# Performance work log

Measured on AMD Instinct MI355X. Metric: run time of the kernel, lower is better.

Reference implementation:

```python
import jax, jax.numpy as jnp
import numpy as np

N, K, H = 50000, 8, 128  # nodes per level, mailbox fanout, hidden size


def setup_inputs() -> dict:
    key = jax.random.key(0)
    ks = jax.random.split(key, 16)
    s = 1.0 / np.sqrt(H)
    inp = {
        "x": jax.random.normal(ks[0], (N, H), jnp.float32),
        "h_mail": jax.random.normal(ks[1], (N, K, H), jnp.float32),
        "c_mail": jax.random.normal(ks[2], (N, K, H), jnp.float32),
        "Wiou": jax.random.uniform(ks[3], (H, 3 * H), jnp.float32, -s, s),
        "Uiou": jax.random.uniform(ks[4], (2 * H, 3 * H), jnp.float32, -s, s),
        "biou": jnp.zeros((1, 3 * H), jnp.float32),
        "Of": jax.random.uniform(ks[5], (H, H), jnp.float32, -s, s),
        "Zf": jax.random.uniform(ks[6], (H, H), jnp.float32, -s, s),
        "Qf": jax.random.uniform(ks[7], (H, H), jnp.float32, -s, s),
        "Kf": jax.random.uniform(ks[8], (H, H), jnp.float32, -s, s),
        "vf": jax.random.uniform(ks[9], (H, H), jnp.float32, -s, s),
        "Wa": jax.random.uniform(ks[10], (H, H), jnp.float32, -s, s),
        "Wd": jax.random.uniform(ks[11], (H, H), jnp.float32, -s, s),
        "Vf": jax.random.uniform(ks[12], (H, 1), jnp.float32, -s, s),
        "etype": jax.random.randint(ks[13], (N, K), 0, 2, jnp.int32),
    }
    return inp


def reference(x, h_mail, c_mail, Wiou, Uiou, biou, Of, Zf, Qf, Kf, vf, Wa, Wd, Vf, etype):
    # --- message: mailbox of child h, c and edge type e (0/1) ---
    e = etype.astype(x.dtype)[..., None]                     # [N,K,1]
    # --- reduce_func ---
    x_tild = x @ Wiou                                        # W_iou(features) -> iou  [N,3H]
    n_tild = x @ Qf                                          # [N,H]
    hk = h_mail @ Kf                                         # K_f(h_tild) [N,K,H]
    v_tild = hk @ vf                                         # [N,K,H]
    w = jax.nn.softmax(jnp.tanh((n_tild[:, None, :] + hk) @ Vf), axis=1)  # [N,K,1]
    modify = jnp.mean(e, axis=1)                             # sum(et)/K  [N,1]
    score_a = (1.0 - modify)[:, None, :]                     # [N,1,1]
    score_b = modify[:, None, :]
    h_til1 = jnp.sum(w * score_a * e * (v_tild @ Wa), axis=1)        # [N,H]
    h_til0 = jnp.sum(w * score_b * (1.0 - e) * (v_tild @ Wd), axis=1)
    h_tild = jnp.concatenate([h_til0, h_til1], axis=1)       # [N,2H]
    f = jax.nn.sigmoid((h_mail * e) @ Of + (h_mail * (1.0 - e)) @ Zf)
    c_red = jnp.sum(f * c_mail, axis=1)                      # [N,H]
    iou = h_tild @ Uiou + x_tild                             # [N,3H]
    # --- apply_node_func ---
    iou = iou + biou
    i, o, u = jnp.split(iou, 3, axis=1)
    i, o, u = jax.nn.sigmoid(i), jax.nn.sigmoid(o), jnp.tanh(u)
    c = i * u + c_red
    h = o * jnp.tanh(c)
    return jnp.stack([h, c])                                 # [2,N,H]
```

## Files before the change

### kernel.cpp

```cpp
#include <hip/hip_runtime.h>
#include <math.h>

#define NN 50000
#define HH 128
#define KK 8

#define WS_WTF  0
#define WS_BT   16384
#define WS_KV   90112
#define WS_T0   106496
#define WS_T1   122880
#define WS_kv   139264
#define WS_qv   139392

typedef __attribute__((ext_vector_type(8))) unsigned short u16x8;
typedef __attribute__((ext_vector_type(8))) __bf16 bf16x8;
typedef __attribute__((ext_vector_type(4))) float f32x4;
union Frag { u16x8 u; bf16x8 b; };

__device__ __forceinline__ unsigned short f2bf(float f) {
    unsigned u = __builtin_bit_cast(unsigned, f);
    u += 0x7fffu + ((u >> 16) & 1u);
    return (unsigned short)(u >> 16);
}
__device__ __forceinline__ float sigm(float v) { return 1.f / (1.f + expf(-v)); }

#define GF(row, slot) ((row) * 128 + ((((slot) ^ ((row) & 7))) << 3))

__global__ void prepA(const float* __restrict__ Kf, const float* __restrict__ Qf,
                      const float* __restrict__ vf, const float* __restrict__ Vf,
                      const float* __restrict__ Wiou, const float* __restrict__ Of,
                      const float* __restrict__ Zf, float* __restrict__ ws) {
    int idx = blockIdx.x * 256 + threadIdx.x;
    unsigned short* bt = (unsigned short*)(ws + WS_BT);
    if (idx < 16384) {
        int a = idx >> 7, c = idx & 127;
        float s = 0.f;
        for (int b = 0; b < 128; ++b) s += Kf[a * 128 + b] * vf[b * 128 + c];
        ws[WS_KV + idx] = s;
    } else if (idx < 16512) {
        int a = idx - 16384;
        float s = 0.f;
        for (int b = 0; b < 128; ++b) s += Kf[a * 128 + b] * Vf[b];
        ws[WS_kv + a] = s;
    } else if (idx < 16640) {
        int a = idx - 16512;
        float s = 0.f;
        for (int b = 0; b < 128; ++b) s += Qf[a * 128 + b] * Vf[b];
        ws[WS_qv + a] = s;
    } else if (idx < 65792) {
        int i = idx - 16640;
        int r = i / 384, c = i % 384;
        bt[c * 384 + r] = f2bf(Wiou[i]);
    } else {
        int i = idx - 65792;
        int c = i >> 8, k = i & 255;
        float v = (k < 128) ? Of[k * 128 + c] : Zf[(k - 128) * 128 + c];
        unsigned short* wtf = (unsigned short*)(ws + WS_WTF);
        wtf[i] = f2bf(v);
    }
}

__global__ void prep2(const float* __restrict__ Wd, const float* __restrict__ Wa,
                      float* __restrict__ ws) {
    int idx = blockIdx.x * 256 + threadIdx.x;
    int sel = idx >> 14;
    int r = (idx >> 7) & 127, c = idx & 127;
    const float* W = sel ? Wa : Wd;
    const float* Kv = ws + WS_KV;
    float s = 0.f;
    for (int h = 0; h < 128; ++h) s += Kv[r * 128 + h] * W[h * 128 + c];
    ws[(sel ? WS_T1 : WS_T0) + r * 128 + c] = s;
}

__global__ void prep3(const float* __restrict__ Uiou, float* __restrict__ ws) {
    int idx = blockIdx.x * 256 + threadIdx.x;
    int half = (idx >= 49152) ? 1 : 0;
    int i2 = idx - half * 49152;
    int r = i2 / 384, c = i2 % 384;
    const float* T = ws + (half ? WS_T1 : WS_T0);
    const float* U = Uiou + half * 128 * 384;
    float s = 0.f;
    for (int h = 0; h < 128; ++h) s += T[r * 128 + h] * U[h * 384 + c];
    unsigned short* bt = (unsigned short*)(ws + WS_BT);
    bt[c * 384 + (128 + half * 128 + r)] = f2bf(s);
}

__global__ __launch_bounds__(256) __attribute__((amdgpu_waves_per_eu(4, 4)))
void tree_main(
    const float* __restrict__ x, const float* __restrict__ h_mail,
    const float* __restrict__ c_mail, const float* __restrict__ biou,
    const int* __restrict__ etype, const float* __restrict__ ws,
    float* __restrict__ out)
{
    __shared__ unsigned short GfS[48 * 128];
    __shared__ float credS[16 * 132];
    __shared__ float efS[128];

    const int t = threadIdx.x;
    const int node0 = blockIdx.x * 16;

    {
        const int n = t >> 4, s = t & 15, c0 = s * 8;
        const int node = node0 + n;
        if (t < 128) efS[t] = (float)etype[node0 * KK + t];

        float xv[8];
        const float4* xp = (const float4*)(x + node * HH + c0);
        float4 x0 = xp[0], x1 = xp[1];
        xv[0]=x0.x; xv[1]=x0.y; xv[2]=x0.z; xv[3]=x0.w;
        xv[4]=x1.x; xv[5]=x1.y; xv[6]=x1.z; xv[7]=x1.w;
        u16x8 xg;
        #pragma unroll
        for (int j = 0; j < 8; ++j) xg[j] = f2bf(xv[j]);
        *(u16x8*)(&GfS[GF(s, n)]) = xg;

        const float4* kvp = (const float4*)(ws + WS_kv + c0);
        float4 k0 = kvp[0], k1 = kvp[1];
        const float4* qvp = (const float4*)(ws + WS_qv + c0);
        float4 q0 = qvp[0], q1 = qvp[1];
        float kvv[8] = {k0.x,k0.y,k0.z,k0.w,k1.x,k1.y,k1.z,k1.w};
        float qvv[8] = {q0.x,q0.y,q0.z,q0.w,q1.x,q1.y,q1.z,q1.w};
        __syncthreads();

        float xq = 0.f;
        #pragma unroll
        for (int j = 0; j < 8; ++j) xq += xv[j] * qvv[j];

        float p[KK];
        #pragma unroll
        for (int k = 0; k < KK; ++k) {
            const float4* hp = (const float4*)(h_mail + (node * KK + k) * HH + c0);
            float4 h0 = hp[0], h1 = hp[1];
            p[k] = h0.x*kvv[0] + h0.y*kvv[1] + h0.z*kvv[2] + h0.w*kvv[3]
                 + h1.x*kvv[4] + h1.y*kvv[5] + h1.z*kvv[6] + h1.w*kvv[7];
        }
        #pragma unroll
        for (int msk = 8; msk >= 1; msk >>= 1) {
            xq += __shfl_xor(xq, msk, 16);
            #pragma unroll
            for (int k = 0; k < KK; ++k) p[k] += __shfl_xor(p[k], msk, 16);
        }
        float ef[KK], esum = 0.f;
        #pragma unroll
        for (int k = 0; k < KK; ++k) { ef[k] = efS[n * KK + k]; esum += ef[k]; }
        const float mod = esum * 0.125f;
        const float sa = 1.f - mod, sb = mod;

        float tk[KK], mx = -1e30f;
        #pragma unroll
        for (int k = 0; k < KK; ++k) { tk[k] = tanhf(xq + p[k]); mx = fmaxf(mx, tk[k]); }
        float wsum = 0.f;
        #pragma unroll
        for (int k = 0; k < KK; ++k) { tk[k] = expf(tk[k] - mx); wsum += tk[k]; }
        const float inv = 1.f / wsum;
        float cf0[KK], cf1[KK];
        #pragma unroll
        for (int k = 0; k < KK; ++k) {
            float w = tk[k] * inv;
            cf0[k] = sb * w * (1.f - ef[k]);
            cf1[k] = sa * w * ef[k];
        }
        float a0[8] = {0,0,0,0,0,0,0,0}, a1[8] = {0,0,0,0,0,0,0,0};
        #pragma unroll
        for (int k = 0; k < KK; ++k) {
            const float4* hp = (const float4*)(h_mail + (node * KK + k) * HH + c0);
            float4 h0 = hp[0], h1 = hp[1];
            float hv[8];
            hv[0]=h0.x; hv[1]=h0.y; hv[2]=h0.z; hv[3]=h0.w;
            hv[4]=h1.x; hv[5]=h1.y; hv[6]=h1.z; hv[7]=h1.w;
            #pragma unroll
            for (int j = 0; j < 8; ++j) { a0[j] += cf0[k]*hv[j]; a1[j] += cf1[k]*hv[j]; }
        }
        u16x8 g0, g1;
        #pragma unroll
        for (int j = 0; j < 8; ++j) { g0[j] = f2bf(a0[j]); g1[j] = f2bf(a1[j]); }
        *(u16x8*)(&GfS[GF(16 + s, n)]) = g0;
        *(u16x8*)(&GfS[GF(32 + s, n)]) = g1;
    }
    __syncthreads();

    const int wave = t >> 6, lane = t & 63, m = lane & 15, q = lane >> 4;
    {
        const unsigned short* WtF = (const unsigned short*)(ws + WS_WTF);
        f32x4 acc[2][8];
        #pragma unroll
        for (int rt = 0; rt < 2; ++rt)
            #pragma unroll
            for (int tc = 0; tc < 8; ++tc) acc[rt][tc] = (f32x4){0.f,0.f,0.f,0.f};

        #pragma unroll
        for (int ks = 0; ks < 8; ++ks) {
            const int kg = ks * 32 + q * 8;
            Frag bf[8], af[2];
            #pragma unroll
            for (int tc = 0; tc < 8; ++tc)
                bf[tc].u = *(const u16x8*)(WtF + (tc * 16 + m) * 256 + kg);
            #pragma unroll
            for (int rt = 0; rt < 2; ++rt) {
                const int r = wave * 32 + rt * 16 + m;
                const float msk = (ks < 4) ? efS[r] : (1.f - efS[r]);
                const float4* hp = (const float4*)(h_mail + (node0 * KK + r) * HH + (kg & 127));
                float4 h0 = hp[0], h1 = hp[1];
                float tv[8];
                tv[0]=h0.x*msk; tv[1]=h0.y*msk; tv[2]=h0.z*msk; tv[3]=h0.w*msk;
                tv[4]=h1.x*msk; tv[5]=h1.y*msk; tv[6]=h1.z*msk; tv[7]=h1.w*msk;
                #pragma unroll
                for (int j = 0; j < 8; ++j) af[rt].u[j] = f2bf(tv[j]);
            }
            #pragma unroll
            for (int rt = 0; rt < 2; ++rt)
                #pragma unroll
                for (int tc = 0; tc < 8; ++tc)
                    acc[rt][tc] = __builtin_amdgcn_mfma_f32_16x16x32_bf16(
                        af[rt].b, bf[tc].b, acc[rt][tc], 0, 0, 0);
        }
        #pragma unroll
        for (int rt = 0; rt < 2; ++rt) {
            const int rbase = wave * 32 + rt * 16;
            const float* cp = c_mail + (node0 * KK + rbase + q * 4) * HH + m;
            float cm[8][4];
            #pragma unroll
            for (int tc = 0; tc < 8; ++tc)
                #pragma unroll
                for (int reg = 0; reg < 4; ++reg)
                    cm[tc][reg] = cp[reg * HH + tc * 16];
            #pragma unroll
            for (int tc = 0; tc < 8; ++tc) {
                float sacc = 0.f;
                #pragma unroll
                for (int reg = 0; reg < 4; ++reg)
                    sacc += sigm(acc[rt][tc][reg]) * cm[tc][reg];
                sacc += __shfl_xor(sacc, 16);
                if ((q & 1) == 0) {
                    const int nl = (rbase >> 3) + (q >> 1);
                    credS[nl * 132 + tc * 16 + m] = sacc;
                }
            }
        }
    }

    f32x4 acc2[6];
    {
        const unsigned short* Bt = (const unsigned short*)(ws + WS_BT);
        #pragma unroll
        for (int j = 0; j < 6; ++j) acc2[j] = (f32x4){0.f,0.f,0.f,0.f};
        #pragma unroll
        for (int ks = 0; ks < 12; ++ks) {
            const int kg = ks * 32 + q * 8;
            const int row = kg >> 3;
            Frag ag;
            ag.u = *(const u16x8*)(&GfS[GF(row, m)]);
            #pragma unroll
            for (int j = 0; j < 6; ++j) {
                const int tile = (j >> 1) * 8 + wave * 2 + (j & 1);
                Frag bg;
                bg.u = *(const u16x8*)(Bt + (tile * 16 + m) * 384 + kg);
                acc2[j] = __builtin_amdgcn_mfma_f32_16x16x32_bf16(
                    ag.b, bg.b, acc2[j], 0, 0, 0);
            }
        }
    }
    __syncthreads();

    {
        #pragma unroll
        for (int jj = 0; jj < 2; ++jj) {
            const int c = (wave * 2 + jj) * 16 + m;
            const float bi = biou[c];
            const float bo = biou[128 + c];
            const float bu = biou[256 + c];
            #pragma unroll
            for (int reg = 0; reg < 4; ++reg) {
                const int n = q * 4 + reg;
                const float ii = sigm(acc2[jj][reg] + bi);
                const float oo = sigm(acc2[2 + jj][reg] + bo);
                const float uu = tanhf(acc2[4 + jj][reg] + bu);
                const float cc = ii * uu + credS[n * 132 + c];
                out[(node0 + n) * HH + c] = oo * tanhf(cc);
                out[NN * HH + (node0 + n) * HH + c] = cc;
            }
        }
    }
}

extern "C" void kernel_launch(void* const* d_in, const int* in_sizes, int n_in,
                              void* d_out, int out_size, void* d_ws, size_t ws_size,
                              hipStream_t stream) {
    const float* x      = (const float*)d_in[0];
    const float* h_mail = (const float*)d_in[1];
    const float* c_mail = (const float*)d_in[2];
    const float* Uiou   = (const float*)d_in[4];
    const float* biou   = (const float*)d_in[5];
    const float* Of     = (const float*)d_in[6];
    const float* Zf     = (const float*)d_in[7];
    const float* Qf     = (const float*)d_in[8];
    const float* Kf     = (const float*)d_in[9];
    const float* vf     = (const float*)d_in[10];
    const float* Wa     = (const float*)d_in[11];
    const float* Wd     = (const float*)d_in[12];
    const float* Vf     = (const float*)d_in[13];
    const int*   etype  = (const int*)d_in[14];
    const float* Wiou   = (const float*)d_in[3];
    float* ws  = (float*)d_ws;
    float* out = (float*)d_out;

    hipLaunchKernelGGL(prepA, dim3(385), dim3(256), 0, stream, Kf, Qf, vf, Vf, Wiou, Of, Zf, ws);
    hipLaunchKernelGGL(prep2, dim3(128), dim3(256), 0, stream, Wd, Wa, ws);
    hipLaunchKernelGGL(prep3, dim3(384), dim3(256), 0, stream, Uiou, ws);
    hipLaunchKernelGGL(tree_main, dim3(3125), dim3(256), 0, stream,
                       x, h_mail, c_mail, biou, etype, ws, out);
}
```

Measured before the change: 884.1 us.

## Fuse three weight-prep kernels into one block-redundant prep kernel and relax main occupancy

Replaces the three chained weight-preparation launches with a single 48-block kernel. Each block recomputes the Kf·vf product into shared memory, multiplies it by Wd or Wa, then produces its own column slice of the folded Uiou weights. This removes two launches and the round trips through global scratch, at the cost of redundant per-block matmul work on few blocks. It also drops the waves_per_eu(4,4) attribute on the main kernel and interleaves the c_mail loads with their use to lower register pressure.

```diff
diff --git a/kernel.cpp b/kernel.cpp
--- a/kernel.cpp
+++ b/kernel.cpp
@@ -7,9 +7,6 @@
 
 #define WS_WTF  0
 #define WS_BT   16384
-#define WS_KV   90112
-#define WS_T0   106496
-#define WS_T1   122880
 #define WS_kv   139264
 #define WS_qv   139392
 
@@ -27,67 +24,78 @@
 
 #define GF(row, slot) ((row) * 128 + ((((slot) ^ ((row) & 7))) << 3))
 
-__global__ void prepA(const float* __restrict__ Kf, const float* __restrict__ Qf,
-                      const float* __restrict__ vf, const float* __restrict__ Vf,
-                      const float* __restrict__ Wiou, const float* __restrict__ Of,
-                      const float* __restrict__ Zf, float* __restrict__ ws) {
-    int idx = blockIdx.x * 256 + threadIdx.x;
-    unsigned short* bt = (unsigned short*)(ws + WS_BT);
-    if (idx < 16384) {
-        int a = idx >> 7, c = idx & 127;
+__global__ __launch_bounds__(512) void prep_all(
+    const float* __restrict__ Kf, const float* __restrict__ Qf,
+    const float* __restrict__ vf, const float* __restrict__ Vf,
+    const float* __restrict__ Wiou, const float* __restrict__ Of,
+    const float* __restrict__ Zf, const float* __restrict__ Wd,
+    const float* __restrict__ Wa, const float* __restrict__ Uiou,
+    float* __restrict__ ws)
+{
+    __shared__ float KVs[128 * 128];
+    const int t = threadIdx.x;
+    const int bh = blockIdx.x;
+    const int half = (bh >= 24) ? 1 : 0;
+    const int cb = (bh % 24) * 16;
+    unsigned short* bt  = (unsigned short*)(ws + WS_BT);
+    unsigned short* wtf = (unsigned short*)(ws + WS_WTF);
+
+    for (int idx = bh * 512 + t; idx < 82176; idx += 48 * 512) {
+        if (idx < 128) {
+            float s = 0.f;
+            for (int b = 0; b < 128; ++b) s += Kf[idx * 128 + b] * Vf[b];
+            ws[WS_kv + idx] = s;
+        } else if (idx < 256) {
+            int a = idx - 128;
+            float s = 0.f;
+            for (int b = 0; b < 128; ++b) s += Qf[a * 128 + b] * Vf[b];
+            ws[WS_qv + a] = s;
+        } else if (idx < 49408) {
+            int i = idx - 256;
+            int r = i / 384, c = i % 384;
+            bt[c * 384 + r] = f2bf(Wiou[i]);
+        } else {
+            int i = idx - 49408;
+            int c = i >> 8, k = i & 255;
+            float v = (k < 128) ? Of[k * 128 + c] : Zf[(k - 128) * 128 + c];
+            wtf[i] = f2bf(v);
+        }
+    }
+
+    for (int i = t; i < 16384; i += 512) {
+        int a = i >> 7, c = i & 127;
         float s = 0.f;
         for (int b = 0; b < 128; ++b) s += Kf[a * 128 + b] * vf[b * 128 + c];
-        ws[WS_KV + idx] = s;
-    } else if (idx < 16512) {
-        int a = idx - 16384;
+        KVs[i] = s;
+    }
+    __syncthreads();
+
+    const float* W = half ? Wa : Wd;
+    float treg[32];
+    #pragma unroll
+    for (int j = 0; j < 32; ++j) {
+        int i = t + j * 512;
+        int r = i >> 7, h = i & 127;
         float s = 0.f;
-        for (int b = 0; b < 128; ++b) s += Kf[a * 128 + b] * Vf[b];
-        ws[WS_kv + a] = s;
-    } else if (idx < 16640) {
-        int a = idx - 16512;
+        for (int g = 0; g < 128; ++g) s += KVs[r * 128 + g] * W[g * 128 + h];
+        treg[j] = s;
+    }
+    __syncthreads();
+    #pragma unroll
+    for (int j = 0; j < 32; ++j) KVs[t + j * 512] = treg[j];
+    __syncthreads();
+
+    const float* U = Uiou + half * 128 * 384;
+    for (int i = t; i < 128 * 16; i += 512) {
+        int r = i >> 4, cc = i & 15;
+        int c = cb + cc;
         float s = 0.f;
-        for (int b = 0; b < 128; ++b) s += Qf[a * 128 + b] * Vf[b];
-        ws[WS_qv + a] = s;
-    } else if (idx < 65792) {
-        int i = idx - 16640;
-        int r = i / 384, c = i % 384;
-        bt[c * 384 + r] = f2bf(Wiou[i]);
-    } else {
-        int i = idx - 65792;
-        int c = i >> 8, k = i & 255;
-        float v = (k < 128) ? Of[k * 128 + c] : Zf[(k - 128) * 128 + c];
-        unsigned short* wtf = (unsigned short*)(ws + WS_WTF);
-        wtf[i] = f2bf(v);
+        for (int h = 0; h < 128; ++h) s += KVs[r * 128 + h] * U[h * 384 + c];
+        bt[c * 384 + (128 + half * 128 + r)] = f2bf(s);
     }
 }
 
-__global__ void prep2(const float* __restrict__ Wd, const float* __restrict__ Wa,
-                      float* __restrict__ ws) {
-    int idx = blockIdx.x * 256 + threadIdx.x;
-    int sel = idx >> 14;
-    int r = (idx >> 7) & 127, c = idx & 127;
-    const float* W = sel ? Wa : Wd;
-    const float* Kv = ws + WS_KV;
-    float s = 0.f;
-    for (int h = 0; h < 128; ++h) s += Kv[r * 128 + h] * W[h * 128 + c];
-    ws[(sel ? WS_T1 : WS_T0) + r * 128 + c] = s;
-}
-
-__global__ void prep3(const float* __restrict__ Uiou, float* __restrict__ ws) {
-    int idx = blockIdx.x * 256 + threadIdx.x;
-    int half = (idx >= 49152) ? 1 : 0;
-    int i2 = idx - half * 49152;
-    int r = i2 / 384, c = i2 % 384;
-    const float* T = ws + (half ? WS_T1 : WS_T0);
-    const float* U = Uiou + half * 128 * 384;
-    float s = 0.f;
-    for (int h = 0; h < 128; ++h) s += T[r * 128 + h] * U[h * 384 + c];
-    unsigned short* bt = (unsigned short*)(ws + WS_BT);
-    bt[c * 384 + (128 + half * 128 + r)] = f2bf(s);
-}
-
-__global__ __launch_bounds__(256) __attribute__((amdgpu_waves_per_eu(4, 4)))
-void tree_main(
+__global__ __launch_bounds__(256) void tree_main(
     const float* __restrict__ x, const float* __restrict__ h_mail,
     const float* __restrict__ c_mail, const float* __restrict__ biou,
     const int* __restrict__ etype, const float* __restrict__ ws,
@@ -219,18 +227,16 @@
         for (int rt = 0; rt < 2; ++rt) {
             const int rbase = wave * 32 + rt * 16;
             const float* cp = c_mail + (node0 * KK + rbase + q * 4) * HH + m;
-            float cm[8][4];
-            #pragma unroll
-            for (int tc = 0; tc < 8; ++tc)
+            #pragma unroll
+            for (int tc = 0; tc < 8; ++tc) {
+                float cm[4];
                 #pragma unroll
                 for (int reg = 0; reg < 4; ++reg)
-                    cm[tc][reg] = cp[reg * HH + tc * 16];
-            #pragma unroll
-            for (int tc = 0; tc < 8; ++tc) {
+                    cm[reg] = cp[reg * HH + tc * 16];
                 float sacc = 0.f;
                 #pragma unroll
                 for (int reg = 0; reg < 4; ++reg)
-                    sacc += sigm(acc[rt][tc][reg]) * cm[tc][reg];
+                    sacc += sigm(acc[rt][tc][reg]) * cm[reg];
                 sacc += __shfl_xor(sacc, 16);
                 if ((q & 1) == 0) {
                     const int nl = (rbase >> 3) + (q >> 1);
@@ -290,6 +296,7 @@
     const float* x      = (const float*)d_in[0];
     const float* h_mail = (const float*)d_in[1];
     const float* c_mail = (const float*)d_in[2];
+    const float* Wiou   = (const float*)d_in[3];
     const float* Uiou   = (const float*)d_in[4];
     const float* biou   = (const float*)d_in[5];
     const float* Of     = (const float*)d_in[6];
@@ -301,13 +308,11 @@
     const float* Wd     = (const float*)d_in[12];
     const float* Vf     = (const float*)d_in[13];
     const int*   etype  = (const int*)d_in[14];
-    const float* Wiou   = (const float*)d_in[3];
     float* ws  = (float*)d_ws;
     float* out = (float*)d_out;
 
-    hipLaunchKernelGGL(prepA, dim3(385), dim3(256), 0, stream, Kf, Qf, vf, Vf, Wiou, Of, Zf, ws);
-    hipLaunchKernelGGL(prep2, dim3(128), dim3(256), 0, stream, Wd, Wa, ws);
-    hipLaunchKernelGGL(prep3, dim3(384), dim3(256), 0, stream, Uiou, ws);
+    hipLaunchKernelGGL(prep_all, dim3(48), dim3(512), 0, stream,
+                       Kf, Qf, vf, Vf, Wiou, Of, Zf, Wd, Wa, Uiou, ws);
     hipLaunchKernelGGL(tree_main, dim3(3125), dim3(256), 0, stream,
                        x, h_mail, c_mail, biou, etype, ws, out);
 }
```

Measured after the change: 915.6 us. +3.6%, slower.
